# Kernel tuning notes

Measured on AMD Instinct MI355X. Metric: run time of the kernel, lower is better.

Reference implementation:

```python
import jax, jax.numpy as jnp
import numpy as np

BN_EPS = 1e-5
K = 2


def _log_shift_max(x):
    # x: [B, C, H, W]. torch.cat([x[..., -s:, :], x[..., :-s, :]], dim=2) == roll(x, +s)
    # and cat([x[..., s:, :], x[..., :s, :]], dim=2) == roll(x, -s).
    H, W = x.shape[2], x.shape[3]
    x_j = jnp.zeros_like(x)
    for i in range(1, int(H).bit_length()):
        s = K ** i - 1
        x_j = jnp.maximum(x_j, x - jnp.roll(x, s, axis=2))
        x_j = jnp.maximum(x_j, x - jnp.roll(x, -s, axis=2))
    for i in range(1, int(W).bit_length()):
        s = K ** i - 1
        x_j = jnp.maximum(x_j, x - jnp.roll(x, s, axis=3))
        x_j = jnp.maximum(x_j, x - jnp.roll(x, -s, axis=3))
    return x_j


def setup_inputs() -> dict:
    key = jax.random.key(0)
    k1, k2 = jax.random.split(key)
    B, C, H, W = 16, 384, 56, 56
    Cout = 384
    x = jax.random.normal(k1, (B, C, H, W), dtype=jnp.float32)
    conv_w = jax.random.normal(k2, (Cout, 2 * C, 1, 1), dtype=jnp.float32) * 0.02
    conv_b = jnp.zeros((Cout,), dtype=jnp.float32)
    bn_scale = jnp.ones((Cout,), dtype=jnp.float32)
    bn_bias = jnp.zeros((Cout,), dtype=jnp.float32)
    bn_mean = jnp.zeros((Cout,), dtype=jnp.float32)
    bn_var = jnp.ones((Cout,), dtype=jnp.float32)
    return {"x": x, "conv_w": conv_w, "conv_b": conv_b,
            "bn_scale": bn_scale, "bn_bias": bn_bias,
            "bn_mean": bn_mean, "bn_var": bn_var}


def reference(x, conv_w, conv_b, bn_scale, bn_bias, bn_mean, bn_var):
    x_j = _log_shift_max(x)                       # [B, C, H, W]
    xc = jnp.concatenate([x, x_j], axis=1)        # [B, 2C, H, W]
    # 1x1 conv == channel contraction
    y = jnp.einsum('bchw,oc->bohw', xc, conv_w[:, :, 0, 0]) + conv_b[None, :, None, None]
    # BatchNorm (eval mode, running stats)
    inv = jax.lax.rsqrt(bn_var + BN_EPS)
    y = (y - bn_mean[None, :, None, None]) * (inv * bn_scale)[None, :, None, None] + bn_bias[None, :, None, None]
    return jax.nn.gelu(y, approximate=False)
```

## Files before the change

kernel.cpp:

```cpp
#include <hip/hip_runtime.h>
#include <cstdint>
#include <cstddef>

typedef unsigned short u16;
typedef unsigned int u32;
typedef __attribute__((ext_vector_type(8))) short short8;
typedef __attribute__((ext_vector_type(4))) float f32x4;

__device__ __forceinline__ float bf2f(u16 v) { return __uint_as_float((u32)v << 16); }
__device__ __forceinline__ u16 f2bf(float f) {
    u32 u = __float_as_uint(f);
    u = (u + 0x7fffu + ((u >> 16) & 1u)) >> 16;
    return (u16)u;
}

#define GLD16(g, l) __builtin_amdgcn_global_load_lds( \
    (const __attribute__((address_space(1))) void*)(g), \
    (__attribute__((address_space(3))) void*)(l), 16, 0, 0)

__global__ void detect_kernel(const u16* __restrict__ x, int* __restrict__ flag) {
    int cnt = 0;
    for (int i = threadIdx.x; i < 256; i += 64) {
        const int e = (x[2 * i] >> 7) & 0xFF;
        cnt += (e >= 96 && e <= 135) ? 1 : 0;
    }
    #pragma unroll
    for (int o = 32; o; o >>= 1) cnt += __shfl_down(cnt, o, 64);
    if (threadIdx.x == 0) *flag = (cnt < 128) ? 1 : 0;
}

__global__ void wconv_kernel(const void* __restrict__ w, u16* __restrict__ wbf,
                             const int* __restrict__ flag) {
    const int i = blockIdx.x * 256 + threadIdx.x;
    if (i >= 384 * 768) return;
    if (*flag) wbf[i] = f2bf(((const float*)w)[i]);
    else       wbf[i] = ((const u16*)w)[i];
}

__global__ __launch_bounds__(512) void xj_kernel(const void* __restrict__ xin,
                                                 u16* __restrict__ xc,
                                                 const int* __restrict__ flag) {
    const int cg = blockIdx.x, b = blockIdx.y;
    const int fp = *flag;
    __shared__ __align__(16) u16 pl[3136][8];
    const size_t plane0 = ((size_t)b * 384 + (size_t)cg * 8) * 3136;

    if (fp) {
        const float* xb = (const float*)xin + plane0;
        for (int g = threadIdx.x; g < 784; g += 512) {
            const int p = g * 4;
            float vv[8][4];
            #pragma unroll
            for (int c = 0; c < 8; ++c) {
                const float4 t = *(const float4*)(xb + (size_t)c * 3136 + p);
                vv[c][0] = t.x; vv[c][1] = t.y; vv[c][2] = t.z; vv[c][3] = t.w;
            }
            #pragma unroll
            for (int i = 0; i < 4; ++i) {
                u32 q[4];
                #pragma unroll
                for (int cc = 0; cc < 4; ++cc)
                    q[cc] = (u32)f2bf(vv[cc * 2][i]) | ((u32)f2bf(vv[cc * 2 + 1][i]) << 16);
                *(uint4*)&pl[p + i][0] = make_uint4(q[0], q[1], q[2], q[3]);
            }
        }
    } else {
        const u16* xb = (const u16*)xin + plane0;
        for (int g = threadIdx.x; g < 784; g += 512) {
            const int p = g * 4;
            u32 rc[8][2];
            #pragma unroll
            for (int c = 0; c < 8; ++c) {
                const uint2 t = *(const uint2*)(xb + (size_t)c * 3136 + p);
                rc[c][0] = t.x; rc[c][1] = t.y;
            }
            #pragma unroll
            for (int i = 0; i < 4; ++i) {
                const int d = i >> 1, sh = (i & 1) * 16;
                u32 q[4];
                #pragma unroll
                for (int cc = 0; cc < 4; ++cc) {
                    const u32 lo = (rc[cc * 2][d] >> sh) & 0xFFFFu;
                    const u32 hi = (rc[cc * 2 + 1][d] >> sh) & 0xFFFFu;
                    q[cc] = lo | (hi << 16);
                }
                *(uint4*)&pl[p + i][0] = make_uint4(q[0], q[1], q[2], q[3]);
            }
        }
    }
    __syncthreads();

    for (int p = threadIdx.x; p < 3136; p += 512) {
        const int h = p / 56, w = p - h * 56;
        const uint4 self = *(const uint4*)&pl[p][0];
        const u32 sw[4] = {self.x, self.y, self.z, self.w};
        float xv[8], mn[8];
        #pragma unroll
        for (int c2 = 0; c2 < 4; ++c2) {
            xv[c2 * 2]     = __uint_as_float(sw[c2] << 16);
            xv[c2 * 2 + 1] = __uint_as_float(sw[c2] & 0xFFFF0000u);
            mn[c2 * 2] = xv[c2 * 2]; mn[c2 * 2 + 1] = xv[c2 * 2 + 1];
        }
        const int S[5] = {1, 3, 7, 15, 31};
        #pragma unroll
        for (int si = 0; si < 5; ++si) {
            const int s = S[si];
            int hp = h + s; if (hp >= 56) hp -= 56;
            int hm = h - s; if (hm < 0)   hm += 56;
            int wp = w + s; if (wp >= 56) wp -= 56;
            int wm = w - s; if (wm < 0)   wm += 56;
            const uint4 n0 = *(const uint4*)&pl[hp * 56 + w][0];
            const uint4 n1 = *(const uint4*)&pl[hm * 56 + w][0];
            const uint4 n2 = *(const uint4*)&pl[h * 56 + wp][0];
            const uint4 n3 = *(const uint4*)&pl[h * 56 + wm][0];
            const u32 w0[4] = {n0.x, n0.y, n0.z, n0.w};
            const u32 w1[4] = {n1.x, n1.y, n1.z, n1.w};
            const u32 w2[4] = {n2.x, n2.y, n2.z, n2.w};
            const u32 w3[4] = {n3.x, n3.y, n3.z, n3.w};
            #pragma unroll
            for (int c2 = 0; c2 < 4; ++c2) {
                mn[c2 * 2] = fminf(
                    fminf(__uint_as_float(w0[c2] << 16), __uint_as_float(w1[c2] << 16)),
                    fminf(fminf(__uint_as_float(w2[c2] << 16), __uint_as_float(w3[c2] << 16)),
                          mn[c2 * 2]));
                mn[c2 * 2 + 1] = fminf(
                    fminf(__uint_as_float(w0[c2] & 0xFFFF0000u), __uint_as_float(w1[c2] & 0xFFFF0000u)),
                    fminf(fminf(__uint_as_float(w2[c2] & 0xFFFF0000u), __uint_as_float(w3[c2] & 0xFFFF0000u)),
                          mn[c2 * 2 + 1]));
            }
        }
        u32 jq[4];
        #pragma unroll
        for (int c2 = 0; c2 < 4; ++c2)
            jq[c2] = (u32)f2bf(xv[c2 * 2] - mn[c2 * 2]) |
                     ((u32)f2bf(xv[c2 * 2 + 1] - mn[c2 * 2 + 1]) << 16);
        u16* px = xc + ((((size_t)b * 96) + cg) * 3136 + p) * 8;
        u16* pj = xc + ((((size_t)b * 96) + 48 + cg) * 3136 + p) * 8;
        *(uint4*)px = self;
        *(uint4*)pj = make_uint4(jq[0], jq[1], jq[2], jq[3]);
    }
}

__global__ __launch_bounds__(256) void gemm_kernel(
        const u16* __restrict__ xc, const u16* __restrict__ Wt,
        const void* __restrict__ cb, const void* __restrict__ bsc,
        const void* __restrict__ bbi, const void* __restrict__ bme,
        const void* __restrict__ bva, void* __restrict__ outp,
        const int* __restrict__ flag) {
    const int ntile = blockIdx.x;
    const int mtile = blockIdx.y;
    const int fp = *flag;
    __shared__ __align__(16) u16 Bs[2][16 * 64 * 8];
    __shared__ float2 PB[192];

    const int tid = threadIdx.x;
    if (tid < 192) {
        const int o = mtile * 192 + tid;
        float vsc, vva, vcb, vme, vbi;
        if (fp) {
            vsc = ((const float*)bsc)[o]; vva = ((const float*)bva)[o];
            vcb = ((const float*)cb)[o];  vme = ((const float*)bme)[o];
            vbi = ((const float*)bbi)[o];
        } else {
            vsc = bf2f(((const u16*)bsc)[o]); vva = bf2f(((const u16*)bva)[o]);
            vcb = bf2f(((const u16*)cb)[o]);  vme = bf2f(((const u16*)bme)[o]);
            vbi = bf2f(((const u16*)bbi)[o]);
        }
        const float seff = vsc * rsqrtf(vva + 1e-5f);
        PB[tid] = make_float2(seff, (vcb - vme) * seff + vbi);
    }

    const int lane = tid & 63, wv = tid >> 6;
    const int quad = lane >> 4, l16 = lane & 15;
    const int bb  = ntile / 49;
    const int hw0 = (ntile - bb * 49) * 64;

    const u16* bgp[4]; int bofs[4];
    #pragma unroll
    for (int i = 0; i < 4; ++i) {
        const int idx = i * 256 + tid;
        const int gg = idx >> 6, n = idx & 63;
        bgp[i]  = xc + (((size_t)bb * 96 + gg) * 3136 + hw0 + n) * 8;
        bofs[i] = idx * 8;
    }
    #define STAGE(q) { \
        u16* dst = &Bs[(q) & 1][0]; \
        _Pragma("unroll") \
        for (int i = 0; i < 4; ++i) GLD16(bgp[i] + (size_t)(q) * 16 * 3136 * 8, dst + bofs[i]); }

    const u16* arow[3];
    #pragma unroll
    for (int im = 0; im < 3; ++im)
        arow[im] = Wt + (size_t)(mtile * 192 + wv * 48 + im * 16 + l16) * 768 + quad * 8;

    f32x4 acc[3][4];
    #pragma unroll
    for (int im = 0; im < 3; ++im)
        #pragma unroll
        for (int in = 0; in < 4; ++in)
            acc[im][in] = {0.f, 0.f, 0.f, 0.f};

    STAGE(0);
    __syncthreads();

    for (int q = 0; q < 6; ++q) {
        if (q < 5) STAGE(q + 1);
        const u16* bufq = &Bs[q & 1][0];
        #pragma unroll
        for (int s = 0; s < 4; ++s) {
            const int k0 = q * 128 + s * 32;
            short8 af[3], bfv[4];
            #pragma unroll
            for (int im = 0; im < 3; ++im)
                af[im] = *(const short8*)(arow[im] + k0);
            #pragma unroll
            for (int in = 0; in < 4; ++in)
                bfv[in] = *(const short8*)(bufq + ((s * 4 + quad) * 64 + in * 16 + l16) * 8);
            #pragma unroll
            for (int im = 0; im < 3; ++im)
                #pragma unroll
                for (int in = 0; in < 4; ++in)
                    acc[im][in] = __builtin_amdgcn_mfma_f32_16x16x32_bf16(
                                      af[im], bfv[in], acc[im][in], 0, 0, 0);
        }
        __syncthreads();
    }

    float* T = (float*)&Bs[0][0] + wv * (16 * 68);
    const size_t obase = (size_t)bb * 384 * 3136 + hw0;
    #pragma unroll
    for (int im = 0; im < 3; ++im) {
        #pragma unroll
        for (int r = 0; r < 4; ++r) {
            const int ml = mtile * 192 + wv * 48 + im * 16 + quad * 4 + r;
            const float2 sb = PB[(wv * 48 + im * 16 + quad * 4 + r)];
            #pragma unroll
            for (int in = 0; in < 4; ++in) {
                float v = acc[im][in][r] * sb.x + sb.y;
                v = 0.5f * v * (1.0f + erff(v * 0.70710678118654752f));
                T[(quad * 4 + r) * 68 + in * 16 + l16] = v;
            }
            (void)ml;
        }
        asm volatile("s_waitcnt lgkmcnt(0)" ::: "memory");
        #pragma unroll
        for (int it = 0; it < 4; ++it) {
            const int flat = it * 256 + lane * 4;
            const int row = flat >> 6, col = flat & 63;
            const float4 vv = *(const float4*)&T[row * 68 + col];
            const size_t oi = obase +
                (size_t)(mtile * 192 + wv * 48 + im * 16 + row) * 3136 + col;
            if (fp) {
                *(float4*)((float*)outp + oi) = vv;
            } else {
                const u32 a = (u32)f2bf(vv.x) | ((u32)f2bf(vv.y) << 16);
                const u32 b2 = (u32)f2bf(vv.z) | ((u32)f2bf(vv.w) << 16);
                *(uint2*)((u16*)outp + oi) = make_uint2(a, b2);
            }
        }
        asm volatile("s_waitcnt lgkmcnt(0)" ::: "memory");
    }
    #undef STAGE
}

extern "C" void kernel_launch(void* const* d_in, const int* in_sizes, int n_in,
                              void* d_out, int out_size, void* d_ws, size_t ws_size,
                              hipStream_t stream) {
    const void* x   = d_in[0];
    const void* w   = d_in[1];
    const void* cbp = d_in[2];
    const void* bsc = d_in[3];
    const void* bbi = d_in[4];
    const void* bme = d_in[5];
    const void* bva = d_in[6];

    int* flag = (int*)d_ws;
    u16* xc   = (u16*)((char*)d_ws + 64);
    u16* wbf  = xc + (size_t)16 * 96 * 3136 * 8;

    detect_kernel<<<1, 64, 0, stream>>>((const u16*)x, flag);
    wconv_kernel<<<1152, 256, 0, stream>>>(w, wbf, flag);
    xj_kernel<<<dim3(48, 16), 512, 0, stream>>>(x, xc, flag);
    gemm_kernel<<<dim3(784, 2), 256, 0, stream>>>(xc, wbf, cbp, bsc, bbi, bme, bva,
                                                  d_out, flag);
}
```

Measured before the change: 269.0 us.

## Merge detect/wconv/xj into one prep kernel and halve GEMM LDS stage size

Removes the separate detect and weight-conversion launches: each block now sniffs the input dtype itself with a wave ballot, and the weight conversion runs in two extra block columns of the x_j prep kernel. The GEMM also recomputes the flag locally and shrinks each double-buffered LDS stage from 128 to 64 K elements, doubling the loop trip count. The goals are fewer launches and less LDS per block, which may allow higher occupancy. The cost is more barriers and smaller prefetch depth in the GEMM, plus redundant dtype sniffing in every block.

After: 258.8 us. 3.8% less time.

```diff
diff --git a/kernel.cpp b/kernel.cpp
--- a/kernel.cpp
+++ b/kernel.cpp
@@ -18,30 +18,35 @@
     (const __attribute__((address_space(1))) void*)(g), \
     (__attribute__((address_space(3))) void*)(l), 16, 0, 0)
 
-__global__ void detect_kernel(const u16* __restrict__ x, int* __restrict__ flag) {
+__device__ __forceinline__ int sniff_fp(const void* x) {
+    const u16* xs = (const u16*)x;
+    const int lane = threadIdx.x & 63;
     int cnt = 0;
-    for (int i = threadIdx.x; i < 256; i += 64) {
-        const int e = (x[2 * i] >> 7) & 0xFF;
-        cnt += (e >= 96 && e <= 135) ? 1 : 0;
-    }
-    #pragma unroll
-    for (int o = 32; o; o >>= 1) cnt += __shfl_down(cnt, o, 64);
-    if (threadIdx.x == 0) *flag = (cnt < 128) ? 1 : 0;
-}
-
-__global__ void wconv_kernel(const void* __restrict__ w, u16* __restrict__ wbf,
-                             const int* __restrict__ flag) {
-    const int i = blockIdx.x * 256 + threadIdx.x;
-    if (i >= 384 * 768) return;
-    if (*flag) wbf[i] = f2bf(((const float*)w)[i]);
-    else       wbf[i] = ((const u16*)w)[i];
-}
-
-__global__ __launch_bounds__(512) void xj_kernel(const void* __restrict__ xin,
-                                                 u16* __restrict__ xc,
-                                                 const int* __restrict__ flag) {
+    #pragma unroll
+    for (int k = 0; k < 4; ++k) {
+        const int i = lane * 4 + k;
+        const int e = (xs[2 * i] >> 7) & 0xFF;
+        cnt += (int)__popcll(__ballot(e >= 96 && e <= 135));
+    }
+    return (cnt < 128) ? 1 : 0;
+}
+
+__global__ __launch_bounds__(512) void prep_kernel(const void* __restrict__ xin,
+                                                   const void* __restrict__ w,
+                                                   u16* __restrict__ xc,
+                                                   u16* __restrict__ wbf) {
     const int cg = blockIdx.x, b = blockIdx.y;
-    const int fp = *flag;
+    const int fp = sniff_fp(xin);
+
+    if (cg >= 48) {
+        const int base = ((cg - 48) * 16 + b) * 512 + threadIdx.x;
+        for (int i = base; i < 384 * 768; i += 32 * 512) {
+            if (fp) wbf[i] = f2bf(((const float*)w)[i]);
+            else    wbf[i] = ((const u16*)w)[i];
+        }
+        return;
+    }
+
     __shared__ __align__(16) u16 pl[3136][8];
     const size_t plane0 = ((size_t)b * 384 + (size_t)cg * 8) * 3136;
 
@@ -91,7 +96,7 @@
     __syncthreads();
 
     for (int p = threadIdx.x; p < 3136; p += 512) {
-        const int h = p / 56, w = p - h * 56;
+        const int h = p / 56, w2 = p - h * 56;
         const uint4 self = *(const uint4*)&pl[p][0];
         const u32 sw[4] = {self.x, self.y, self.z, self.w};
         float xv[8], mn[8];
@@ -107,25 +112,25 @@
             const int s = S[si];
             int hp = h + s; if (hp >= 56) hp -= 56;
             int hm = h - s; if (hm < 0)   hm += 56;
-            int wp = w + s; if (wp >= 56) wp -= 56;
-            int wm = w - s; if (wm < 0)   wm += 56;
-            const uint4 n0 = *(const uint4*)&pl[hp * 56 + w][0];
-            const uint4 n1 = *(const uint4*)&pl[hm * 56 + w][0];
+            int wp = w2 + s; if (wp >= 56) wp -= 56;
+            int wm = w2 - s; if (wm < 0)   wm += 56;
+            const uint4 n0 = *(const uint4*)&pl[hp * 56 + w2][0];
+            const uint4 n1 = *(const uint4*)&pl[hm * 56 + w2][0];
             const uint4 n2 = *(const uint4*)&pl[h * 56 + wp][0];
             const uint4 n3 = *(const uint4*)&pl[h * 56 + wm][0];
             const u32 w0[4] = {n0.x, n0.y, n0.z, n0.w};
             const u32 w1[4] = {n1.x, n1.y, n1.z, n1.w};
-            const u32 w2[4] = {n2.x, n2.y, n2.z, n2.w};
-            const u32 w3[4] = {n3.x, n3.y, n3.z, n3.w};
+            const u32 wA[4] = {n2.x, n2.y, n2.z, n2.w};
+            const u32 wB[4] = {n3.x, n3.y, n3.z, n3.w};
             #pragma unroll
             for (int c2 = 0; c2 < 4; ++c2) {
                 mn[c2 * 2] = fminf(
                     fminf(__uint_as_float(w0[c2] << 16), __uint_as_float(w1[c2] << 16)),
-                    fminf(fminf(__uint_as_float(w2[c2] << 16), __uint_as_float(w3[c2] << 16)),
+                    fminf(fminf(__uint_as_float(wA[c2] << 16), __uint_as_float(wB[c2] << 16)),
                           mn[c2 * 2]));
                 mn[c2 * 2 + 1] = fminf(
                     fminf(__uint_as_float(w0[c2] & 0xFFFF0000u), __uint_as_float(w1[c2] & 0xFFFF0000u)),
-                    fminf(fminf(__uint_as_float(w2[c2] & 0xFFFF0000u), __uint_as_float(w3[c2] & 0xFFFF0000u)),
+                    fminf(fminf(__uint_as_float(wA[c2] & 0xFFFF0000u), __uint_as_float(wB[c2] & 0xFFFF0000u)),
                           mn[c2 * 2 + 1]));
             }
         }
@@ -146,12 +151,13 @@
         const void* __restrict__ cb, const void* __restrict__ bsc,
         const void* __restrict__ bbi, const void* __restrict__ bme,
         const void* __restrict__ bva, void* __restrict__ outp,
-        const int* __restrict__ flag) {
+        const void* __restrict__ x0) {
     const int ntile = blockIdx.x;
     const int mtile = blockIdx.y;
-    const int fp = *flag;
-    __shared__ __align__(16) u16 Bs[2][16 * 64 * 8];
+    const int fp = sniff_fp(x0);
+    __shared__ __align__(16) unsigned char smem[17408];
     __shared__ float2 PB[192];
+    u16* const Bsu = (u16*)smem;
 
     const int tid = threadIdx.x;
     if (tid < 192) {
@@ -175,18 +181,18 @@
     const int bb  = ntile / 49;
     const int hw0 = (ntile - bb * 49) * 64;
 
-    const u16* bgp[4]; int bofs[4];
-    #pragma unroll
-    for (int i = 0; i < 4; ++i) {
+    const u16* bgp[2]; int bofs[2];
+    #pragma unroll
+    for (int i = 0; i < 2; ++i) {
         const int idx = i * 256 + tid;
         const int gg = idx >> 6, n = idx & 63;
         bgp[i]  = xc + (((size_t)bb * 96 + gg) * 3136 + hw0 + n) * 8;
         bofs[i] = idx * 8;
     }
     #define STAGE(q) { \
-        u16* dst = &Bs[(q) & 1][0]; \
+        u16* dst = Bsu + ((q) & 1) * 4096; \
         _Pragma("unroll") \
-        for (int i = 0; i < 4; ++i) GLD16(bgp[i] + (size_t)(q) * 16 * 3136 * 8, dst + bofs[i]); }
+        for (int i = 0; i < 2; ++i) GLD16(bgp[i] + (size_t)(q) * 8 * 3136 * 8, dst + bofs[i]); }
 
     const u16* arow[3];
     #pragma unroll
@@ -203,12 +209,12 @@
     STAGE(0);
     __syncthreads();
 
-    for (int q = 0; q < 6; ++q) {
-        if (q < 5) STAGE(q + 1);
-        const u16* bufq = &Bs[q & 1][0];
-        #pragma unroll
-        for (int s = 0; s < 4; ++s) {
-            const int k0 = q * 128 + s * 32;
+    for (int q = 0; q < 12; ++q) {
+        if (q < 11) STAGE(q + 1);
+        const u16* bufq = Bsu + (q & 1) * 4096;
+        #pragma unroll
+        for (int s = 0; s < 2; ++s) {
+            const int k0 = q * 64 + s * 32;
             short8 af[3], bfv[4];
             #pragma unroll
             for (int im = 0; im < 3; ++im)
@@ -226,13 +232,12 @@
         __syncthreads();
     }
 
-    float* T = (float*)&Bs[0][0] + wv * (16 * 68);
+    float* T = (float*)smem + wv * (16 * 68);
     const size_t obase = (size_t)bb * 384 * 3136 + hw0;
     #pragma unroll
     for (int im = 0; im < 3; ++im) {
         #pragma unroll
         for (int r = 0; r < 4; ++r) {
-            const int ml = mtile * 192 + wv * 48 + im * 16 + quad * 4 + r;
             const float2 sb = PB[(wv * 48 + im * 16 + quad * 4 + r)];
             #pragma unroll
             for (int in = 0; in < 4; ++in) {
@@ -240,7 +245,6 @@
                 v = 0.5f * v * (1.0f + erff(v * 0.70710678118654752f));
                 T[(quad * 4 + r) * 68 + in * 16 + l16] = v;
             }
-            (void)ml;
         }
         asm volatile("s_waitcnt lgkmcnt(0)" ::: "memory");
         #pragma unroll
@@ -274,13 +278,10 @@
     const void* bme = d_in[5];
     const void* bva = d_in[6];
 
-    int* flag = (int*)d_ws;
     u16* xc   = (u16*)((char*)d_ws + 64);
     u16* wbf  = xc + (size_t)16 * 96 * 3136 * 8;
 
-    detect_kernel<<<1, 64, 0, stream>>>((const u16*)x, flag);
-    wconv_kernel<<<1152, 256, 0, stream>>>(w, wbf, flag);
-    xj_kernel<<<dim3(48, 16), 512, 0, stream>>>(x, xc, flag);
+    prep_kernel<<<dim3(50, 16), 512, 0, stream>>>(x, w, xc, wbf);
     gemm_kernel<<<dim3(784, 2), 256, 0, stream>>>(xc, wbf, cbp, bsc, bbi, bme, bva,
-                                                  d_out, flag);
-}
+                                                  d_out, x);
+}
```
